# Kernel tuning notes

Measured on AMD Instinct MI355X. Metric: run time of the kernel, lower is better.

The kernel has to match this reference:

```python
import jax, jax.numpy as jnp
import numpy as np

N, IN_SZ, OUT_SZ = 8192, 512, 64

def setup_inputs() -> dict:
    key = jax.random.key(0)
    ks = jax.random.split(key, 7)
    s_in = 1.0 / np.sqrt(IN_SZ)
    inp = {
        "input": jax.random.normal(ks[0], (N, IN_SZ), dtype=jnp.float32),
        "Wq": jax.random.uniform(ks[1], (OUT_SZ, IN_SZ), jnp.float32, -s_in, s_in),
        "bq": jax.random.uniform(ks[2], (OUT_SZ,), jnp.float32, -s_in, s_in),
        "Wk": jax.random.uniform(ks[3], (OUT_SZ, IN_SZ), jnp.float32, -s_in, s_in),
        "bk": jax.random.uniform(ks[4], (OUT_SZ,), jnp.float32, -s_in, s_in),
        "Wv": jax.random.uniform(ks[5], (OUT_SZ, IN_SZ), jnp.float32, -s_in, s_in),
        "bv": jax.random.uniform(ks[6], (OUT_SZ,), jnp.float32, -s_in, s_in),
    }
    return inp

def reference(input, Wq, bq, Wk, bk, Wv, bv):
    # torch nn.Linear: x @ W.T + b
    q = input @ Wq.T + bq  # [N, out]
    k = input @ Wk.T + bk  # [N, out]
    v = input @ Wv.T + bv  # [N, out]
    # NOTE: original module has NO 1/sqrt(d) scaling.
    scores = jax.nn.softmax(q @ k.T, axis=-1)  # [N, N]
    return scores @ v  # [N, out]
```

## Files before the change

### kernel.cpp

```cpp
#include <hip/hip_runtime.h>
#include <math.h>

#define SA_N   8192
#define SA_IN  512
#define SA_D   64
#define G_SPL  16

typedef short s16x8 __attribute__((ext_vector_type(8)));
typedef float f32x16 __attribute__((ext_vector_type(16)));

#define MFMA32(A, B, C) __builtin_amdgcn_mfma_f32_32x32x16_bf16((A), (B), (C), 0, 0, 0)

static __device__ __forceinline__ unsigned short f2bf_rn(float x) {
    unsigned int u = __float_as_uint(x);
    unsigned int r = (u + 0x7FFFu + ((u >> 16) & 1u)) >> 16;
    return (unsigned short)r;
}

static __device__ __forceinline__ void trunc_split(float f, unsigned short* hi, unsigned short* lo) {
    unsigned int u = __float_as_uint(f);
    *hi = (unsigned short)(u >> 16);
    float lf = f - __uint_as_float(u & 0xFFFF0000u);
    *lo = (unsigned short)(__float_as_uint(lf) >> 16);
}

static __device__ __forceinline__ void split8(const float4 a, const float4 b, s16x8* xh, s16x8* xl) {
    union { unsigned int u[4]; s16x8 v; } H, L;
    const float f[8] = {a.x, a.y, a.z, a.w, b.x, b.y, b.z, b.w};
#pragma unroll
    for (int p = 0; p < 4; ++p) {
        const unsigned int u0 = __float_as_uint(f[2 * p]);
        const unsigned int u1 = __float_as_uint(f[2 * p + 1]);
        H.u[p] = (u0 >> 16) | (u1 & 0xFFFF0000u);
        const float l0 = f[2 * p]     - __uint_as_float(u0 & 0xFFFF0000u);
        const float l1 = f[2 * p + 1] - __uint_as_float(u1 & 0xFFFF0000u);
        L.u[p] = (__float_as_uint(l0) >> 16) | (__float_as_uint(l1) & 0xFFFF0000u);
    }
    *xh = H.v; *xl = L.v;
}

__global__ __launch_bounds__(256) void wconv_kernel(
    const float* __restrict__ Wq, const float* __restrict__ Wk, const float* __restrict__ Wv,
    unsigned short* __restrict__ WHI, unsigned short* __restrict__ WLO)
{
    const int idx  = blockIdx.x * 256 + threadIdx.x;
    const int mat  = idx >> 15;
    const int rem  = idx & 32767;
    const int mt   = rem >> 14;
    const int ks   = (rem >> 9) & 31;
    const int lane = (rem >> 3) & 63;
    const int i    = rem & 7;
    const int o = mt * 32 + (lane & 31);
    const int k = ks * 16 + (lane >> 5) * 8 + i;
    const float* W = (mat == 0) ? Wq : (mat == 1 ? Wk : Wv);
    unsigned short hi, lo;
    trunc_split(W[o * SA_IN + k], &hi, &lo);
    WHI[idx] = hi; WLO[idx] = lo;
}

__global__ __launch_bounds__(512, 2) void qkv_kernel(
    const float* __restrict__ in,
    const unsigned short* __restrict__ WHI, const unsigned short* __restrict__ WLO,
    const float* __restrict__ bq, const float* __restrict__ bk, const float* __restrict__ bv,
    unsigned short* __restrict__ Qhi, unsigned short* __restrict__ Qlo,
    unsigned short* __restrict__ KhiF, unsigned short* __restrict__ KloF,
    unsigned short* __restrict__ VF)
{
    __shared__ float cbuf[8][64][20];
    __shared__ __align__(16) unsigned short stage[5 * 2048];
    const int t    = threadIdx.x;
    const int w    = t >> 6;
    const int lane = t & 63;
    const int h    = lane >> 5;
    const int q32  = lane & 31;
    const int jt   = blockIdx.x;
    const int rows0 = jt * 32;

    const s16x8* WH8 = (const s16x8*)WHI;
    const s16x8* WL8 = (const s16x8*)WLO;

    f32x16 acc[6] = {};

#pragma unroll
    for (int ksl = 0; ksl < 4; ++ksl) {
        const int ks = (w << 2) + ksl;
        const float* xp = in + (size_t)(rows0 + q32) * SA_IN + ks * 16 + h * 8;
        const float4 xa = *(const float4*)xp;
        const float4 xb = *(const float4*)(xp + 4);
        s16x8 xh, xl;
        split8(xa, xb, &xh, &xl);
        const int fb = ks * 64 + lane;
#pragma unroll
        for (int mt = 0; mt < 2; ++mt) {
            s16x8 ah = WH8[(0 + mt) * 2048 + fb];
            s16x8 al = WL8[(0 + mt) * 2048 + fb];
            acc[mt] = MFMA32(ah, xh, acc[mt]);
            acc[mt] = MFMA32(ah, xl, acc[mt]);
            acc[mt] = MFMA32(al, xh, acc[mt]);
            ah = WH8[(2 + mt) * 2048 + fb];
            al = WL8[(2 + mt) * 2048 + fb];
            acc[2 + mt] = MFMA32(ah, xh, acc[2 + mt]);
            acc[2 + mt] = MFMA32(ah, xl, acc[2 + mt]);
            acc[2 + mt] = MFMA32(al, xh, acc[2 + mt]);
            ah = WH8[(4 + mt) * 2048 + fb];
            acc[4 + mt] = MFMA32(ah, xh, acc[4 + mt]);
        }
    }

#pragma unroll
    for (int s = 0; s < 6; ++s) {
        __syncthreads();
#pragma unroll
        for (int rg = 0; rg < 4; ++rg) {
            float4 vv = { acc[s][4 * rg + 0], acc[s][4 * rg + 1],
                          acc[s][4 * rg + 2], acc[s][4 * rg + 3] };
            *(float4*)&cbuf[w][lane][4 * rg] = vv;
        }
        __syncthreads();
        if (w == s) {
            const int mat = s >> 1;
            const int mt  = s & 1;
            float c[16];
#pragma unroll
            for (int rg = 0; rg < 4; ++rg) {
                float4 acc4 = *(const float4*)&cbuf[0][lane][4 * rg];
#pragma unroll
                for (int p = 1; p < 8; ++p) {
                    const float4 pp = *(const float4*)&cbuf[p][lane][4 * rg];
                    acc4.x += pp.x; acc4.y += pp.y; acc4.z += pp.z; acc4.w += pp.w;
                }
                c[4 * rg + 0] = acc4.x; c[4 * rg + 1] = acc4.y;
                c[4 * rg + 2] = acc4.z; c[4 * rg + 3] = acc4.w;
            }
            const float* B = (mat == 0) ? bq : (mat == 1 ? bk : bv);
#pragma unroll
            for (int r = 0; r < 16; ++r) {
                const int o = mt * 32 + (r & 3) + 8 * (r >> 2) + 4 * h;
                const float val = c[r] + B[o];
                if (mat == 0) {
                    unsigned short hi, lo;
                    trunc_split(val, &hi, &lo);
                    stage[0    + q32 * 64 + o] = hi;
                    stage[2048 + q32 * 64 + o] = lo;
                } else if (mat == 1) {
                    unsigned short hi, lo;
                    trunc_split(val, &hi, &lo);
                    const int kl_ = ((o >> 4) * 64 + ((o >> 3) & 1) * 32 + q32) * 8 + (o & 7);
                    stage[4096 + kl_] = hi;
                    stage[6144 + kl_] = lo;
                } else {
                    const int vl_ = ((o >> 5) * 2 + ((q32 >> 4) & 1)) * 512
                                  + ((q32 >> 3) & 1) * 256 + (o & 31) * 8 + (q32 & 7);
                    stage[8192 + vl_] = f2bf_rn(val);
                }
            }
        }
    }
    __syncthreads();

    {
        const uint4* st4 = (const uint4*)stage;
        for (int i = t; i < 1280; i += 512) {
            const int r = i >> 8;
            const int off = (i & 255) * 8;
            unsigned short* dst =
                (r == 0) ? Qhi  + (size_t)rows0 * 64 :
                (r == 1) ? Qlo  + (size_t)rows0 * 64 :
                (r == 2) ? KhiF + (size_t)jt * 2048 :
                (r == 3) ? KloF + (size_t)jt * 2048 :
                           VF   + (size_t)jt * 2048;
            *(uint4*)(dst + off) = st4[i];
        }
    }
}

__global__ __launch_bounds__(256, 2) void attn_kernel(
    const unsigned short* __restrict__ Qhi, const unsigned short* __restrict__ Qlo,
    const unsigned short* __restrict__ KhiF, const unsigned short* __restrict__ KloF,
    const unsigned short* __restrict__ VF,
    unsigned short* __restrict__ Opart, float* __restrict__ Lpart)
{
    const int t    = threadIdx.x;
    const int w    = t >> 6;
    const int lane = t & 63;
    const int h    = lane >> 5;
    const int q32  = lane & 31;
    const int qb   = blockIdx.x >> 4;
    const int g    = blockIdx.x & 15;
    const int q0   = (qb * 4 + w) * 32;

    s16x8 qh[4], ql[4];
#pragma unroll
    for (int s = 0; s < 4; ++s) {
        const size_t off = (size_t)(q0 + q32) * 64 + s * 16 + h * 8;
        qh[s] = *reinterpret_cast<const s16x8*>(Qhi + off);
        ql[s] = *reinterpret_cast<const s16x8*>(Qlo + off);
    }

    const s16x8* KH = reinterpret_cast<const s16x8*>(KhiF);
    const s16x8* KL = reinterpret_cast<const s16x8*>(KloF);
    const s16x8* VV = reinterpret_cast<const s16x8*>(VF);

    f32x16 O0 = {}, O1 = {};
    float lsum = 0.f;

    auto process = [&](const s16x8* kh, const s16x8* kl, const s16x8* vv) {
        f32x16 S = {};
#pragma unroll
        for (int s = 0; s < 4; ++s) S = MFMA32(kh[s], qh[s], S);
#pragma unroll
        for (int s = 0; s < 4; ++s) S = MFMA32(kh[s], ql[s], S);
#pragma unroll
        for (int s = 0; s < 4; ++s) S = MFMA32(kl[s], qh[s], S);

        float e[16];
#pragma unroll
        for (int r = 0; r < 16; ++r) e[r] = __expf(S[r]);
        lsum += (((e[0] + e[1]) + (e[2] + e[3])) + ((e[4] + e[5]) + (e[6] + e[7])))
              + (((e[8] + e[9]) + (e[10] + e[11])) + ((e[12] + e[13]) + (e[14] + e[15])));

        unsigned int pk[8];
#pragma unroll
        for (int j2 = 0; j2 < 8; ++j2)
            pk[j2] = (__float_as_uint(e[2 * j2]) >> 16) | (__float_as_uint(e[2 * j2 + 1]) & 0xFFFF0000u);

        unsigned int x[8];
#pragma unroll
        for (int j2 = 0; j2 < 8; ++j2) x[j2] = (unsigned int)__shfl_xor((int)pk[j2], 32, 64);

        union { unsigned int u[4]; s16x8 v; } P0, P1;
        P0.u[0] = h ? x[2]  : pk[0];
        P0.u[1] = h ? x[3]  : pk[1];
        P0.u[2] = h ? pk[2] : x[0];
        P0.u[3] = h ? pk[3] : x[1];
        P1.u[0] = h ? x[6]  : pk[4];
        P1.u[1] = h ? x[7]  : pk[5];
        P1.u[2] = h ? pk[6] : x[4];
        P1.u[3] = h ? pk[7] : x[5];

        O0 = MFMA32(vv[0], P0.v, O0);
        O0 = MFMA32(vv[1], P1.v, O0);
        O1 = MFMA32(vv[2], P0.v, O1);
        O1 = MFMA32(vv[3], P1.v, O1);
    };

    for (int it = 0; it < 16; it += 2) {
        const int jtA = g * 16 + it;
        const int jtB = jtA + 1;
        s16x8 khA[4], klA[4], vA[4], khB[4], klB[4], vB[4];
#pragma unroll
        for (int s = 0; s < 4; ++s) {
            khA[s] = KH[(jtA * 4 + s) * 64 + lane];
            klA[s] = KL[(jtA * 4 + s) * 64 + lane];
            vA[s]  = VV[(jtA * 4 + s) * 64 + lane];
            khB[s] = KH[(jtB * 4 + s) * 64 + lane];
            klB[s] = KL[(jtB * 4 + s) * 64 + lane];
            vB[s]  = VV[(jtB * 4 + s) * 64 + lane];
        }
        process(khA, klA, vA);
        process(khB, klB, vB);
    }

    lsum += __shfl_xor(lsum, 32, 64);

    const size_t qg = (size_t)g * SA_N + q0 + q32;
#pragma unroll
    for (int rg = 0; rg < 4; ++rg) {
        const int d0 = 8 * rg + 4 * h;
        uint2 s0, s1;
        s0.x = (unsigned int)f2bf_rn(O0[4 * rg + 0]) | ((unsigned int)f2bf_rn(O0[4 * rg + 1]) << 16);
        s0.y = (unsigned int)f2bf_rn(O0[4 * rg + 2]) | ((unsigned int)f2bf_rn(O0[4 * rg + 3]) << 16);
        s1.x = (unsigned int)f2bf_rn(O1[4 * rg + 0]) | ((unsigned int)f2bf_rn(O1[4 * rg + 1]) << 16);
        s1.y = (unsigned int)f2bf_rn(O1[4 * rg + 2]) | ((unsigned int)f2bf_rn(O1[4 * rg + 3]) << 16);
        *(uint2*)(Opart + qg * 64 + d0)      = s0;
        *(uint2*)(Opart + qg * 64 + d0 + 32) = s1;
    }
    if (h == 0) Lpart[qg] = lsum;
}

__global__ __launch_bounds__(256) void combine_kernel(
    const unsigned short* __restrict__ Opart, const float* __restrict__ Lpart,
    float* __restrict__ out)
{
    const int tid = blockIdx.x * 256 + threadIdx.x;
    const int q  = tid >> 5;
    const int dp = tid & 31;
    const unsigned int* OP = (const unsigned int*)Opart;
    float s0 = 0.f, s1 = 0.f, lt = 0.f;
#pragma unroll
    for (int g = 0; g < G_SPL; ++g) {
        const unsigned int v = OP[((size_t)g * SA_N + q) * 32 + dp];
        s0 += __uint_as_float(v << 16);
        s1 += __uint_as_float(v & 0xFFFF0000u);
        lt += Lpart[(size_t)g * SA_N + q];
    }
    float2 r = { s0 / lt, s1 / lt };
    *(float2*)&out[(size_t)q * 64 + dp * 2] = r;
}

extern "C" void kernel_launch(void* const* d_in, const int* in_sizes, int n_in,
                              void* d_out, int out_size, void* d_ws, size_t ws_size,
                              hipStream_t stream) {
    const float* input = (const float*)d_in[0];
    const float* Wq    = (const float*)d_in[1];
    const float* bq    = (const float*)d_in[2];
    const float* Wk    = (const float*)d_in[3];
    const float* bk    = (const float*)d_in[4];
    const float* Wv    = (const float*)d_in[5];
    const float* bv    = (const float*)d_in[6];
    float* out = (float*)d_out;

    const size_t SEG = (size_t)SA_N * 64;
    unsigned short* WHI  = (unsigned short*)d_ws;
    unsigned short* WLO  = WHI  + 98304;
    unsigned short* Qhi  = WLO  + 98304;
    unsigned short* Qlo  = Qhi  + SEG;
    unsigned short* KhiF = Qlo  + SEG;
    unsigned short* KloF = KhiF + SEG;
    unsigned short* VF   = KloF + SEG;
    unsigned short* Opart = VF  + SEG;
    float*          Lpart = (float*)(Opart + (size_t)G_SPL * SA_N * 64);

    wconv_kernel<<<384, 256, 0, stream>>>(Wq, Wk, Wv, WHI, WLO);
    qkv_kernel<<<256, 512, 0, stream>>>(input, WHI, WLO, bq, bk, bv,
                                        Qhi, Qlo, KhiF, KloF, VF);
    attn_kernel<<<64 * G_SPL, 256, 0, stream>>>(Qhi, Qlo, KhiF, KloF, VF, Opart, Lpart);
    combine_kernel<<<1024, 256, 0, stream>>>(Opart, Lpart, out);
}
```

Baseline: 141.4 us.

## Fuse weight conversion into QKV projection and split attention score MFMA chains

Removes the separate weight-split kernel and converts fp32 weights to bf16 hi/lo inside the QKV kernel, which now runs one block per (matrix, row tile) with 256 threads. This trims cross-warp reduction to four partials and shrinks the shared staging buffer. In attention, the three dependent score MFMA chains become three independent accumulators that are summed before exp, to expose MFMA pipeline parallelism. In exchange, each block re-reads and re-splits the weights, and the input rows are read three times.

```diff
diff --git a/kernel.cpp b/kernel.cpp
--- a/kernel.cpp
+++ b/kernel.cpp
@@ -39,120 +39,115 @@
     *xh = H.v; *xl = L.v;
 }
 
-__global__ __launch_bounds__(256) void wconv_kernel(
-    const float* __restrict__ Wq, const float* __restrict__ Wk, const float* __restrict__ Wv,
-    unsigned short* __restrict__ WHI, unsigned short* __restrict__ WLO)
-{
-    const int idx  = blockIdx.x * 256 + threadIdx.x;
-    const int mat  = idx >> 15;
-    const int rem  = idx & 32767;
-    const int mt   = rem >> 14;
-    const int ks   = (rem >> 9) & 31;
-    const int lane = (rem >> 3) & 63;
-    const int i    = rem & 7;
-    const int o = mt * 32 + (lane & 31);
-    const int k = ks * 16 + (lane >> 5) * 8 + i;
-    const float* W = (mat == 0) ? Wq : (mat == 1 ? Wk : Wv);
-    unsigned short hi, lo;
-    trunc_split(W[o * SA_IN + k], &hi, &lo);
-    WHI[idx] = hi; WLO[idx] = lo;
-}
-
-__global__ __launch_bounds__(512, 2) void qkv_kernel(
+static __device__ __forceinline__ s16x8 pack_rn8(const float4 a, const float4 b) {
+    union { unsigned int u[4]; s16x8 v; } P;
+    const float f[8] = {a.x, a.y, a.z, a.w, b.x, b.y, b.z, b.w};
+#pragma unroll
+    for (int p = 0; p < 4; ++p)
+        P.u[p] = (unsigned int)f2bf_rn(f[2 * p]) | ((unsigned int)f2bf_rn(f[2 * p + 1]) << 16);
+    return P.v;
+}
+
+__global__ __launch_bounds__(256, 2) void qkv_kernel(
     const float* __restrict__ in,
-    const unsigned short* __restrict__ WHI, const unsigned short* __restrict__ WLO,
-    const float* __restrict__ bq, const float* __restrict__ bk, const float* __restrict__ bv,
+    const float* __restrict__ Wq, const float* __restrict__ bq,
+    const float* __restrict__ Wk, const float* __restrict__ bk,
+    const float* __restrict__ Wv, const float* __restrict__ bv,
     unsigned short* __restrict__ Qhi, unsigned short* __restrict__ Qlo,
     unsigned short* __restrict__ KhiF, unsigned short* __restrict__ KloF,
     unsigned short* __restrict__ VF)
 {
-    __shared__ float cbuf[8][64][20];
-    __shared__ __align__(16) unsigned short stage[5 * 2048];
+    __shared__ float cbuf[2][4][64][20];
+    __shared__ __align__(16) unsigned short stage[4096];
     const int t    = threadIdx.x;
     const int w    = t >> 6;
     const int lane = t & 63;
     const int h    = lane >> 5;
     const int q32  = lane & 31;
-    const int jt   = blockIdx.x;
+    const int mat  = blockIdx.x >> 8;
+    const int jt   = blockIdx.x & 255;
     const int rows0 = jt * 32;
 
-    const s16x8* WH8 = (const s16x8*)WHI;
-    const s16x8* WL8 = (const s16x8*)WLO;
-
-    f32x16 acc[6] = {};
-
-#pragma unroll
-    for (int ksl = 0; ksl < 4; ++ksl) {
-        const int ks = (w << 2) + ksl;
+    const float* W = (mat == 0) ? Wq : (mat == 1 ? Wk : Wv);
+    const float* B = (mat == 0) ? bq : (mat == 1 ? bk : bv);
+
+    f32x16 accA[2] = {};
+    f32x16 accB[2] = {};
+
+#pragma unroll 2
+    for (int ksl = 0; ksl < 8; ++ksl) {
+        const int ks = (w << 3) + ksl;
         const float* xp = in + (size_t)(rows0 + q32) * SA_IN + ks * 16 + h * 8;
         const float4 xa = *(const float4*)xp;
         const float4 xb = *(const float4*)(xp + 4);
         s16x8 xh, xl;
         split8(xa, xb, &xh, &xl);
-        const int fb = ks * 64 + lane;
 #pragma unroll
         for (int mt = 0; mt < 2; ++mt) {
-            s16x8 ah = WH8[(0 + mt) * 2048 + fb];
-            s16x8 al = WL8[(0 + mt) * 2048 + fb];
-            acc[mt] = MFMA32(ah, xh, acc[mt]);
-            acc[mt] = MFMA32(ah, xl, acc[mt]);
-            acc[mt] = MFMA32(al, xh, acc[mt]);
-            ah = WH8[(2 + mt) * 2048 + fb];
-            al = WL8[(2 + mt) * 2048 + fb];
-            acc[2 + mt] = MFMA32(ah, xh, acc[2 + mt]);
-            acc[2 + mt] = MFMA32(ah, xl, acc[2 + mt]);
-            acc[2 + mt] = MFMA32(al, xh, acc[2 + mt]);
-            ah = WH8[(4 + mt) * 2048 + fb];
-            acc[4 + mt] = MFMA32(ah, xh, acc[4 + mt]);
-        }
-    }
-
-#pragma unroll
-    for (int s = 0; s < 6; ++s) {
-        __syncthreads();
+            const float* wp = W + (size_t)(mt * 32 + q32) * SA_IN + ks * 16 + h * 8;
+            const float4 wa = *(const float4*)wp;
+            const float4 wb = *(const float4*)(wp + 4);
+            if (mat < 2) {
+                s16x8 ah, al;
+                split8(wa, wb, &ah, &al);
+                accA[mt] = MFMA32(ah, xh, accA[mt]);
+                accB[mt] = MFMA32(ah, xl, accB[mt]);
+                accA[mt] = MFMA32(al, xh, accA[mt]);
+            } else {
+                const s16x8 ah = pack_rn8(wa, wb);
+                accA[mt] = MFMA32(ah, xh, accA[mt]);
+            }
+        }
+    }
+
+#pragma unroll
+    for (int mt = 0; mt < 2; ++mt) {
+        f32x16 tot = accA[mt];
+        if (mat < 2) {
+#pragma unroll
+            for (int r = 0; r < 16; ++r) tot[r] += accB[mt][r];
+        }
 #pragma unroll
         for (int rg = 0; rg < 4; ++rg) {
-            float4 vv = { acc[s][4 * rg + 0], acc[s][4 * rg + 1],
-                          acc[s][4 * rg + 2], acc[s][4 * rg + 3] };
-            *(float4*)&cbuf[w][lane][4 * rg] = vv;
-        }
-        __syncthreads();
-        if (w == s) {
-            const int mat = s >> 1;
-            const int mt  = s & 1;
-            float c[16];
-#pragma unroll
-            for (int rg = 0; rg < 4; ++rg) {
-                float4 acc4 = *(const float4*)&cbuf[0][lane][4 * rg];
-#pragma unroll
-                for (int p = 1; p < 8; ++p) {
-                    const float4 pp = *(const float4*)&cbuf[p][lane][4 * rg];
-                    acc4.x += pp.x; acc4.y += pp.y; acc4.z += pp.z; acc4.w += pp.w;
-                }
-                c[4 * rg + 0] = acc4.x; c[4 * rg + 1] = acc4.y;
-                c[4 * rg + 2] = acc4.z; c[4 * rg + 3] = acc4.w;
-            }
-            const float* B = (mat == 0) ? bq : (mat == 1 ? bk : bv);
-#pragma unroll
-            for (int r = 0; r < 16; ++r) {
-                const int o = mt * 32 + (r & 3) + 8 * (r >> 2) + 4 * h;
-                const float val = c[r] + B[o];
-                if (mat == 0) {
-                    unsigned short hi, lo;
-                    trunc_split(val, &hi, &lo);
-                    stage[0    + q32 * 64 + o] = hi;
-                    stage[2048 + q32 * 64 + o] = lo;
-                } else if (mat == 1) {
-                    unsigned short hi, lo;
-                    trunc_split(val, &hi, &lo);
-                    const int kl_ = ((o >> 4) * 64 + ((o >> 3) & 1) * 32 + q32) * 8 + (o & 7);
-                    stage[4096 + kl_] = hi;
-                    stage[6144 + kl_] = lo;
-                } else {
-                    const int vl_ = ((o >> 5) * 2 + ((q32 >> 4) & 1)) * 512
-                                  + ((q32 >> 3) & 1) * 256 + (o & 31) * 8 + (q32 & 7);
-                    stage[8192 + vl_] = f2bf_rn(val);
-                }
+            float4 vv = { tot[4 * rg + 0], tot[4 * rg + 1],
+                          tot[4 * rg + 2], tot[4 * rg + 3] };
+            *(float4*)&cbuf[mt][w][lane][4 * rg] = vv;
+        }
+    }
+    __syncthreads();
+    if (w < 2) {
+        const int mt = w;
+        float c[16];
+#pragma unroll
+        for (int rg = 0; rg < 4; ++rg) {
+            const float4 s0 = *(const float4*)&cbuf[mt][0][lane][4 * rg];
+            const float4 s1 = *(const float4*)&cbuf[mt][1][lane][4 * rg];
+            const float4 s2 = *(const float4*)&cbuf[mt][2][lane][4 * rg];
+            const float4 s3 = *(const float4*)&cbuf[mt][3][lane][4 * rg];
+            c[4 * rg + 0] = (s0.x + s1.x) + (s2.x + s3.x);
+            c[4 * rg + 1] = (s0.y + s1.y) + (s2.y + s3.y);
+            c[4 * rg + 2] = (s0.z + s1.z) + (s2.z + s3.z);
+            c[4 * rg + 3] = (s0.w + s1.w) + (s2.w + s3.w);
+        }
+#pragma unroll
+        for (int r = 0; r < 16; ++r) {
+            const int o = mt * 32 + (r & 3) + 8 * (r >> 2) + 4 * h;
+            const float val = c[r] + B[o];
+            if (mat == 0) {
+                unsigned short hi, lo;
+                trunc_split(val, &hi, &lo);
+                stage[q32 * 64 + o]        = hi;
+                stage[2048 + q32 * 64 + o] = lo;
+            } else if (mat == 1) {
+                unsigned short hi, lo;
+                trunc_split(val, &hi, &lo);
+                const int kl_ = ((o >> 4) * 64 + ((o >> 3) & 1) * 32 + q32) * 8 + (o & 7);
+                stage[kl_]        = hi;
+                stage[2048 + kl_] = lo;
+            } else {
+                const int vl_ = ((o >> 5) * 2 + ((q32 >> 4) & 1)) * 512
+                              + ((q32 >> 3) & 1) * 256 + (o & 31) * 8 + (q32 & 7);
+                stage[vl_] = f2bf_rn(val);
             }
         }
     }
@@ -160,16 +155,18 @@
 
     {
         const uint4* st4 = (const uint4*)stage;
-        for (int i = t; i < 1280; i += 512) {
-            const int r = i >> 8;
-            const int off = (i & 255) * 8;
-            unsigned short* dst =
-                (r == 0) ? Qhi  + (size_t)rows0 * 64 :
-                (r == 1) ? Qlo  + (size_t)rows0 * 64 :
-                (r == 2) ? KhiF + (size_t)jt * 2048 :
-                (r == 3) ? KloF + (size_t)jt * 2048 :
-                           VF   + (size_t)jt * 2048;
-            *(uint4*)(dst + off) = st4[i];
+        if (mat == 0) {
+            for (int i = t; i < 512; i += 256) {
+                unsigned short* dst = ((i < 256) ? Qhi : Qlo) + (size_t)rows0 * 64 + (i & 255) * 8;
+                *(uint4*)dst = st4[i];
+            }
+        } else if (mat == 1) {
+            for (int i = t; i < 512; i += 256) {
+                unsigned short* dst = ((i < 256) ? KhiF : KloF) + (size_t)jt * 2048 + (i & 255) * 8;
+                *(uint4*)dst = st4[i];
+            }
+        } else {
+            *(uint4*)(VF + (size_t)jt * 2048 + t * 8) = st4[t];
         }
     }
 }
@@ -205,17 +202,17 @@
     float lsum = 0.f;
 
     auto process = [&](const s16x8* kh, const s16x8* kl, const s16x8* vv) {
-        f32x16 S = {};
-#pragma unroll
-        for (int s = 0; s < 4; ++s) S = MFMA32(kh[s], qh[s], S);
-#pragma unroll
-        for (int s = 0; s < 4; ++s) S = MFMA32(kh[s], ql[s], S);
-#pragma unroll
-        for (int s = 0; s < 4; ++s) S = MFMA32(kl[s], qh[s], S);
+        f32x16 Sa = {}, Sb = {}, Sc = {};
+#pragma unroll
+        for (int s = 0; s < 4; ++s) {
+            Sa = MFMA32(kh[s], qh[s], Sa);
+            Sb = MFMA32(kh[s], ql[s], Sb);
+            Sc = MFMA32(kl[s], qh[s], Sc);
+        }
 
         float e[16];
 #pragma unroll
-        for (int r = 0; r < 16; ++r) e[r] = __expf(S[r]);
+        for (int r = 0; r < 16; ++r) e[r] = __expf((Sa[r] + Sb[r]) + Sc[r]);
         lsum += (((e[0] + e[1]) + (e[2] + e[3])) + ((e[4] + e[5]) + (e[6] + e[7])))
               + (((e[8] + e[9]) + (e[10] + e[11])) + ((e[12] + e[13]) + (e[14] + e[15])));
 
@@ -311,9 +308,7 @@
     float* out = (float*)d_out;
 
     const size_t SEG = (size_t)SA_N * 64;
-    unsigned short* WHI  = (unsigned short*)d_ws;
-    unsigned short* WLO  = WHI  + 98304;
-    unsigned short* Qhi  = WLO  + 98304;
+    unsigned short* Qhi  = (unsigned short*)d_ws;
     unsigned short* Qlo  = Qhi  + SEG;
     unsigned short* KhiF = Qlo  + SEG;
     unsigned short* KloF = KhiF + SEG;
@@ -321,8 +316,7 @@
     unsigned short* Opart = VF  + SEG;
     float*          Lpart = (float*)(Opart + (size_t)G_SPL * SA_N * 64);
 
-    wconv_kernel<<<384, 256, 0, stream>>>(Wq, Wk, Wv, WHI, WLO);
-    qkv_kernel<<<256, 512, 0, stream>>>(input, WHI, WLO, bq, bk, bv,
+    qkv_kernel<<<768, 256, 0, stream>>>(input, Wq, bq, Wk, bk, Wv, bv,
                                         Qhi, Qlo, KhiF, KloF, VF);
     attn_kernel<<<64 * G_SPL, 256, 0, stream>>>(Qhi, Qlo, KhiF, KloF, VF, Opart, Lpart);
     combine_kernel<<<1024, 256, 0, stream>>>(Opart, Lpart, out);
```

Result: slower. 146.9 us (+3.9%).
